# Kernel tuning notes

Hardware: AMD Instinct MI355X
Metric: run time of the kernel (lower is better)

Reference implementation:

```python
import jax, jax.numpy as jnp
import numpy as np

# LJ / module constants (from init_kwargs / defaults)
C = 1.0
RC = 1.0
P = 12
Q = 6
GAMMA = 0.1
MIN_R = 0.1

N_NODES = 100000
N_EDGES = 3200000
DIM = 3


def setup_inputs() -> dict:
    key = jax.random.key(0)
    k1, k2, k3, k4 = jax.random.split(key, 4)
    x = jax.random.normal(k1, (N_NODES, DIM), dtype=jnp.float32)
    v = jax.random.normal(k2, (N_NODES, DIM), dtype=jnp.float32)
    src = jax.random.randint(k3, (N_EDGES,), 0, N_NODES, dtype=jnp.int64)
    dst = jax.random.randint(k4, (N_EDGES,), 0, N_NODES, dtype=jnp.int64)
    return {"x": x, "v": v, "src": src, "dst": dst, "n_nodes": N_NODES}


def lj_force(r_in):
    # clamp r at MIN_R:  r = r_in if r_in > MIN_R else MIN_R
    r = jnp.where(r_in > MIN_R, r_in, MIN_R)
    s = RC / r
    return 4.0 * C * s**Q * (P * s**(P - Q) - Q) / r


def reference(x, v, src, dst, n_nodes):
    # gather edge endpoint positions; non-periodic distance: dst - src
    dr = x[dst] - x[src]                                  # [E, D]
    abs_dr = jnp.linalg.norm(dr, axis=-1, keepdims=True)  # [E, 1]
    # F.normalize(dr, dim=-1) -> dr / max(||dr||, eps)
    unit_dr = dr / jnp.maximum(abs_dr, 1e-12)             # [E, D]
    msg = lj_force(abs_dr) * unit_dr                      # [E, D]
    # scatter-sum messages into destination nodes
    acc = jax.ops.segment_sum(msg, dst, num_segments=n_nodes)  # [N, D]
    return acc - GAMMA * v
```

## Files before the change

kernel.cpp:

```cpp
#include <hip/hip_runtime.h>

#define GAMMA 0.1f
#define MIN_R 0.1f

#define NR 256
#define LOG_NR 8
#define RMAXB 512
#define SC_BS 4096
#define THR_S 512
#define THR_B 512
#define CAP 9216
#define NBMAX 1024

typedef unsigned int u32;

__device__ __forceinline__ u32 wave_incl_scan(u32 x) {
    #pragma unroll
    for (int d = 1; d < 64; d <<= 1) {
        u32 y = __shfl_up(x, d);
        if ((int)(threadIdx.x & 63) >= d) x += y;
    }
    return x;
}

__device__ __forceinline__ void lj_accum(float4 xd, float4 xs,
                                         float& ax, float& ay, float& az)
{
    float dx = xd.x - xs.x, dy = xd.y - xs.y, dz = xd.z - xs.z;
    float r2 = dx * dx + dy * dy + dz * dz;
    float rr = sqrtf(r2);
    float inv_norm = 1.0f / fmaxf(rr, 1e-12f);
    float rc = fmaxf(rr, MIN_R);
    float s1 = 1.0f / rc;
    float s2 = s1 * s1;
    float s6 = s2 * s2 * s2;
    float F = 4.0f * s6 * (12.0f * s6 - 6.0f) * s1;
    float sc = F * inv_norm;
    ax += sc * dx; ay += sc * dy; az += sc * dz;
}

__global__ __launch_bounds__(THR_S) void scatter_kernel(
    const float* __restrict__ x, const int* __restrict__ src,
    const int* __restrict__ dst, float4* __restrict__ xp,
    u32* __restrict__ pk1, u32* __restrict__ tab,
    int n_nodes, int n_edges, int NBv, int R)
{
    __shared__ u32 payload[SC_BS];
    __shared__ u32 hist[RMAXB], loff[RMAXB], lcur[RMAXB];
    __shared__ u32 wsb[8];
    const int b = blockIdx.x, t = threadIdx.x;

    for (int i = b * THR_S + t; i < n_nodes; i += NBv * THR_S)
        xp[i] = make_float4(x[3 * i + 0], x[3 * i + 1], x[3 * i + 2], 0.0f);

    const int s0 = b * SC_BS;
    const int n  = min(SC_BS, n_edges - s0);
    const int lim = s0 + n;

    hist[t] = 0u;
    __syncthreads();

    for (int e = s0 + t * 4; e < lim; e += THR_S * 4) {
        if (e + 3 < lim) {
            int4 d4 = *(const int4*)(dst + e);
            atomicAdd(&hist[(u32)d4.x >> LOG_NR], 1u);
            atomicAdd(&hist[(u32)d4.y >> LOG_NR], 1u);
            atomicAdd(&hist[(u32)d4.z >> LOG_NR], 1u);
            atomicAdd(&hist[(u32)d4.w >> LOG_NR], 1u);
        } else {
            for (int q = e; q < lim; ++q)
                atomicAdd(&hist[(u32)dst[q] >> LOG_NR], 1u);
        }
    }
    __syncthreads();

    {
        u32 h = hist[t];
        u32 inc = wave_incl_scan(h);
        if ((t & 63) == 63) wsb[t >> 6] = inc;
        __syncthreads();
        u32 pre = 0;
        #pragma unroll
        for (int w = 0; w < 8; ++w) if (w < (t >> 6)) pre += wsb[w];
        u32 ex = pre + inc - h;
        loff[t] = ex; lcur[t] = ex;
    }
    __syncthreads();

    for (int e = s0 + t * 4; e < lim; e += THR_S * 4) {
        if (e + 3 < lim) {
            int4 d4 = *(const int4*)(dst + e);
            int4 s4 = *(const int4*)(src + e);
            #pragma unroll
            for (int q = 0; q < 4; ++q) {
                u32 d = (u32)((q == 0) ? d4.x : (q == 1) ? d4.y : (q == 2) ? d4.z : d4.w);
                u32 sv = (u32)((q == 0) ? s4.x : (q == 1) ? s4.y : (q == 2) ? s4.z : s4.w);
                u32 r = d >> LOG_NR;
                u32 w = ((d & (NR - 1)) << 17) | sv;
                u32 slot = atomicAdd(&lcur[r], 1u);
                payload[slot] = w;
            }
        } else {
            for (int q = e; q < lim; ++q) {
                u32 d = (u32)dst[q];
                u32 sv = (u32)src[q];
                u32 r = d >> LOG_NR;
                u32 w = ((d & (NR - 1)) << 17) | sv;
                u32 slot = atomicAdd(&lcur[r], 1u);
                payload[slot] = w;
            }
        }
    }
    __syncthreads();

    for (int j = t; j < n; j += THR_S) pk1[s0 + j] = payload[j];
    for (int i = t; i < R; i += THR_S)
        tab[(size_t)b * R + i] = (loff[i] << 13) | hist[i];
}

__global__ __launch_bounds__(THR_B, 4) void binprocess_kernel(
    const float4* __restrict__ xp, const u32* __restrict__ pk1,
    const u32* __restrict__ tab, const float* __restrict__ v,
    float* __restrict__ out, int n_nodes, int NBv, int R)
{
    __shared__ u32 buf[CAP];
    __shared__ u32 sorted[CAP];
    __shared__ u32 segoff[NBMAX];
    __shared__ u32 hist[NR], cur[NR], ns[NR];
    __shared__ u32 wsb[8];
    __shared__ u32 shv[2];
    const int r = blockIdx.x, t = threadIdx.x;

    u32 c0 = 0, c1 = 0;
    if (t < NBv) c0 = tab[(size_t)t * R + r] & 8191u;
    if (t + THR_B < NBv) c1 = tab[(size_t)(t + THR_B) * R + r] & 8191u;
    u32 inc0 = wave_incl_scan(c0);
    if ((t & 63) == 63) wsb[t >> 6] = inc0;
    __syncthreads();
    u32 pre0 = 0;
    #pragma unroll
    for (int w = 0; w < 8; ++w) if (w < (t >> 6)) pre0 += wsb[w];
    u32 s0i = pre0 + inc0;
    if (t == THR_B - 1) shv[0] = s0i;
    __syncthreads();
    const u32 T0 = shv[0];
    u32 inc1 = wave_incl_scan(c1);
    if ((t & 63) == 63) wsb[t >> 6] = inc1;
    __syncthreads();
    u32 pre1 = 0;
    #pragma unroll
    for (int w = 0; w < 8; ++w) if (w < (t >> 6)) pre1 += wsb[w];
    u32 s1i = pre1 + inc1;
    if (t < NBv) segoff[t] = s0i - c0;
    if (t + THR_B < NBv) segoff[t + THR_B] = T0 + s1i - c1;
    if (t == THR_B - 1) shv[1] = T0 + s1i;
    __syncthreads();
    const u32 total = shv[1];

    if (total <= CAP) {
        if (t < NR) hist[t] = 0u;
        __syncthreads();
        for (int j = t; j < NBv; j += THR_B) {
            u32 w = tab[(size_t)j * R + r];
            int cnt = (int)(w & 8191u);
            const u32* seg = pk1 + (size_t)j * SC_BS + (w >> 13);
            u32 base = segoff[j];
            int k = 0;
            for (; k + 3 < cnt; k += 4) {
                u32 w0 = seg[k], w1 = seg[k + 1], w2 = seg[k + 2], w3 = seg[k + 3];
                buf[base + k] = w0; buf[base + k + 1] = w1;
                buf[base + k + 2] = w2; buf[base + k + 3] = w3;
                atomicAdd(&hist[w0 >> 17], 1u);
                atomicAdd(&hist[w1 >> 17], 1u);
                atomicAdd(&hist[w2 >> 17], 1u);
                atomicAdd(&hist[w3 >> 17], 1u);
            }
            for (; k < cnt; ++k) {
                u32 w0 = seg[k];
                buf[base + k] = w0;
                atomicAdd(&hist[w0 >> 17], 1u);
            }
        }
        __syncthreads();

        {
            u32 h = (t < NR) ? hist[t] : 0u;
            u32 inc = wave_incl_scan(h);
            if ((t & 63) == 63) wsb[t >> 6] = inc;
            __syncthreads();
            u32 pre = 0;
            #pragma unroll
            for (int w = 0; w < 8; ++w) if (w < (t >> 6)) pre += wsb[w];
            if (t < NR) {
                u32 ex = pre + inc - h;
                ns[t] = ex; cur[t] = ex;
            }
        }
        __syncthreads();

        for (int i = t; i < (int)total; i += THR_B) {
            u32 w = buf[i];
            u32 p = atomicAdd(&cur[w >> 17], 1u);
            sorted[p] = w & 0x1FFFFu;
        }
        __syncthreads();

        const int dl = t >> 1, half = t & 1;
        const int node = (r << LOG_NR) + dl;
        if (node < n_nodes) {
            const float4 xd = xp[node];
            const int ee0 = (int)ns[dl];
            const int ee1 = (dl < NR - 1) ? (int)ns[dl + 1] : (int)total;
            float ax = 0.f, ay = 0.f, az = 0.f;
            int e = ee0 + half;
            for (; e + 6 < ee1; e += 8) {
                u32 q0 = sorted[e], q1 = sorted[e + 2];
                u32 q2 = sorted[e + 4], q3 = sorted[e + 6];
                float4 a0 = xp[q0], a1 = xp[q1], a2 = xp[q2], a3 = xp[q3];
                lj_accum(xd, a0, ax, ay, az);
                lj_accum(xd, a1, ax, ay, az);
                lj_accum(xd, a2, ax, ay, az);
                lj_accum(xd, a3, ax, ay, az);
            }
            for (; e < ee1; e += 2) {
                float4 a = xp[sorted[e]];
                lj_accum(xd, a, ax, ay, az);
            }
            ax += __shfl_xor(ax, 1);
            ay += __shfl_xor(ay, 1);
            az += __shfl_xor(az, 1);
            if (half == 0) {
                out[3 * node + 0] = ax - GAMMA * v[3 * node + 0];
                out[3 * node + 1] = ay - GAMMA * v[3 * node + 1];
                out[3 * node + 2] = az - GAMMA * v[3 * node + 2];
            }
        }
    } else {
        float* acc = (float*)buf;
        for (int i = t; i < NR * 3; i += THR_B) acc[i] = 0.f;
        __syncthreads();
        for (int j = t; j < NBv; j += THR_B) {
            u32 w = tab[(size_t)j * R + r];
            int cnt = (int)(w & 8191u);
            const u32* seg = pk1 + (size_t)j * SC_BS + (w >> 13);
            for (int k = 0; k < cnt; ++k) {
                u32 w0 = seg[k];
                int u = (int)(w0 >> 17);
                int node = (r << LOG_NR) + u;
                float4 xs = xp[w0 & 0x1FFFFu];
                float4 xd = xp[node];
                float ax = 0.f, ay = 0.f, az = 0.f;
                lj_accum(xd, xs, ax, ay, az);
                unsafeAtomicAdd(&acc[3 * u + 0], ax);
                unsafeAtomicAdd(&acc[3 * u + 1], ay);
                unsafeAtomicAdd(&acc[3 * u + 2], az);
            }
        }
        __syncthreads();
        for (int i = t; i < NR; i += THR_B) {
            int node = (r << LOG_NR) + i;
            if (node < n_nodes) {
                out[3 * node + 0] = acc[3 * i + 0] - GAMMA * v[3 * node + 0];
                out[3 * node + 1] = acc[3 * i + 1] - GAMMA * v[3 * node + 1];
                out[3 * node + 2] = acc[3 * i + 2] - GAMMA * v[3 * node + 2];
            }
        }
    }
}

__global__ void init_out_kernel(const float* __restrict__ v,
                                float* __restrict__ out, int n) {
    int i = blockIdx.x * blockDim.x + threadIdx.x;
    if (i < n) out[i] = -GAMMA * v[i];
}

__global__ void edge_atomic_kernel(const float* __restrict__ x,
                                   const int* __restrict__ src,
                                   const int* __restrict__ dst,
                                   float* __restrict__ out, int n_edges) {
    int e = blockIdx.x * blockDim.x + threadIdx.x;
    if (e < n_edges) {
        const int s3 = 3 * src[e], d3 = 3 * dst[e];
        float dx = x[d3 + 0] - x[s3 + 0];
        float dy = x[d3 + 1] - x[s3 + 1];
        float dz = x[d3 + 2] - x[s3 + 2];
        float r2 = dx * dx + dy * dy + dz * dz;
        float rr = sqrtf(r2);
        float inv_norm = 1.0f / fmaxf(rr, 1e-12f);
        float rc = fmaxf(rr, MIN_R);
        float s1 = 1.0f / rc;
        float s2 = s1 * s1;
        float s6 = s2 * s2 * s2;
        float F = 4.0f * s6 * (12.0f * s6 - 6.0f) * s1;
        float sc = F * inv_norm;
        unsafeAtomicAdd(&out[d3 + 0], sc * dx);
        unsafeAtomicAdd(&out[d3 + 1], sc * dy);
        unsafeAtomicAdd(&out[d3 + 2], sc * dz);
    }
}

extern "C" void kernel_launch(void* const* d_in, const int* in_sizes, int n_in,
                              void* d_out, int out_size, void* d_ws, size_t ws_size,
                              hipStream_t stream) {
    const float* x   = (const float*)d_in[0];
    const float* v   = (const float*)d_in[1];
    const int*   src = (const int*)d_in[2];
    const int*   dst = (const int*)d_in[3];
    float* out = (float*)d_out;

    const int n_out   = out_size;
    const int n_nodes = out_size / 3;
    const int n_edges = in_sizes[2];
    const int R   = (n_nodes + NR - 1) / NR;
    const int NBv = (n_edges + SC_BS - 1) / SC_BS;

    size_t off = 0;
    auto take = [&off](size_t bytes) {
        size_t o = off;
        off = (off + bytes + 63) & ~(size_t)63;
        return o;
    };
    const size_t xp_o  = take((size_t)n_nodes * 16);
    const size_t tab_o = take((size_t)NBv * R * 4);
    const size_t pk1_o = take((size_t)NBv * SC_BS * 4);
    const size_t need = off;

    const int blk = 256;
    if (n_nodes <= (1 << 17) && R <= RMAXB && NBv <= NBMAX && need <= ws_size) {
        float4* xp = (float4*)((char*)d_ws + xp_o);
        u32* tab   = (u32*)((char*)d_ws + tab_o);
        u32* pk1   = (u32*)((char*)d_ws + pk1_o);

        scatter_kernel<<<NBv, THR_S, 0, stream>>>(x, src, dst, xp, pk1, tab,
                                                  n_nodes, n_edges, NBv, R);
        binprocess_kernel<<<R, THR_B, 0, stream>>>(xp, pk1, tab, v, out,
                                                   n_nodes, NBv, R);
    } else {
        init_out_kernel<<<(n_out + blk - 1) / blk, blk, 0, stream>>>(v, out, n_out);
        edge_atomic_kernel<<<(n_edges + blk - 1) / blk, blk, 0, stream>>>(
            x, src, dst, out, n_edges);
    }
}
```

Before: 115.3 us.

## Transpose bin table, drop staging buffer, and register-cache edges in scatter

```diff
diff --git a/kernel.cpp b/kernel.cpp
--- a/kernel.cpp
+++ b/kernel.cpp
@@ -10,7 +10,6 @@
 #define THR_S 512
 #define THR_B 512
 #define CAP 9216
-#define NBMAX 1024
 
 typedef unsigned int u32;
 
@@ -39,7 +38,7 @@
     ax += sc * dx; ay += sc * dy; az += sc * dz;
 }
 
-__global__ __launch_bounds__(THR_S) void scatter_kernel(
+__global__ __launch_bounds__(THR_S, 4) void scatter_kernel(
     const float* __restrict__ x, const int* __restrict__ src,
     const int* __restrict__ dst, float4* __restrict__ xp,
     u32* __restrict__ pk1, u32* __restrict__ tab,
@@ -57,21 +56,49 @@
     const int n  = min(SC_BS, n_edges - s0);
     const int lim = s0 + n;
 
+    u32 da[8], sa[8];
+    bool va[8];
+    {
+        const int eA = s0 + t * 4;
+        const int eB = eA + THR_S * 4;
+        if (eA + 3 < lim) {
+            int4 d4 = *(const int4*)(dst + eA);
+            int4 s4 = *(const int4*)(src + eA);
+            da[0] = (u32)d4.x; da[1] = (u32)d4.y; da[2] = (u32)d4.z; da[3] = (u32)d4.w;
+            sa[0] = (u32)s4.x; sa[1] = (u32)s4.y; sa[2] = (u32)s4.z; sa[3] = (u32)s4.w;
+            va[0] = va[1] = va[2] = va[3] = true;
+        } else {
+            #pragma unroll
+            for (int q = 0; q < 4; ++q) {
+                int qe = eA + q;
+                va[q] = qe < lim;
+                da[q] = va[q] ? (u32)dst[qe] : 0u;
+                sa[q] = va[q] ? (u32)src[qe] : 0u;
+            }
+        }
+        if (eB + 3 < lim) {
+            int4 d4 = *(const int4*)(dst + eB);
+            int4 s4 = *(const int4*)(src + eB);
+            da[4] = (u32)d4.x; da[5] = (u32)d4.y; da[6] = (u32)d4.z; da[7] = (u32)d4.w;
+            sa[4] = (u32)s4.x; sa[5] = (u32)s4.y; sa[6] = (u32)s4.z; sa[7] = (u32)s4.w;
+            va[4] = va[5] = va[6] = va[7] = true;
+        } else {
+            #pragma unroll
+            for (int q = 0; q < 4; ++q) {
+                int qe = eB + q;
+                va[4 + q] = qe < lim;
+                da[4 + q] = va[4 + q] ? (u32)dst[qe] : 0u;
+                sa[4 + q] = va[4 + q] ? (u32)src[qe] : 0u;
+            }
+        }
+    }
+
     hist[t] = 0u;
     __syncthreads();
 
-    for (int e = s0 + t * 4; e < lim; e += THR_S * 4) {
-        if (e + 3 < lim) {
-            int4 d4 = *(const int4*)(dst + e);
-            atomicAdd(&hist[(u32)d4.x >> LOG_NR], 1u);
-            atomicAdd(&hist[(u32)d4.y >> LOG_NR], 1u);
-            atomicAdd(&hist[(u32)d4.z >> LOG_NR], 1u);
-            atomicAdd(&hist[(u32)d4.w >> LOG_NR], 1u);
-        } else {
-            for (int q = e; q < lim; ++q)
-                atomicAdd(&hist[(u32)dst[q] >> LOG_NR], 1u);
-        }
-    }
+    #pragma unroll
+    for (int q = 0; q < 8; ++q)
+        if (va[q]) atomicAdd(&hist[da[q] >> LOG_NR], 1u);
     __syncthreads();
 
     {
@@ -87,35 +114,19 @@
     }
     __syncthreads();
 
-    for (int e = s0 + t * 4; e < lim; e += THR_S * 4) {
-        if (e + 3 < lim) {
-            int4 d4 = *(const int4*)(dst + e);
-            int4 s4 = *(const int4*)(src + e);
-            #pragma unroll
-            for (int q = 0; q < 4; ++q) {
-                u32 d = (u32)((q == 0) ? d4.x : (q == 1) ? d4.y : (q == 2) ? d4.z : d4.w);
-                u32 sv = (u32)((q == 0) ? s4.x : (q == 1) ? s4.y : (q == 2) ? s4.z : s4.w);
-                u32 r = d >> LOG_NR;
-                u32 w = ((d & (NR - 1)) << 17) | sv;
-                u32 slot = atomicAdd(&lcur[r], 1u);
-                payload[slot] = w;
-            }
-        } else {
-            for (int q = e; q < lim; ++q) {
-                u32 d = (u32)dst[q];
-                u32 sv = (u32)src[q];
-                u32 r = d >> LOG_NR;
-                u32 w = ((d & (NR - 1)) << 17) | sv;
-                u32 slot = atomicAdd(&lcur[r], 1u);
-                payload[slot] = w;
-            }
+    #pragma unroll
+    for (int q = 0; q < 8; ++q) {
+        if (va[q]) {
+            u32 r = da[q] >> LOG_NR;
+            u32 w = ((da[q] & (NR - 1)) << 17) | sa[q];
+            u32 slot = atomicAdd(&lcur[r], 1u);
+            payload[slot] = w;
         }
     }
     __syncthreads();
 
     for (int j = t; j < n; j += THR_S) pk1[s0 + j] = payload[j];
-    for (int i = t; i < R; i += THR_S)
-        tab[(size_t)b * R + i] = (loff[i] << 13) | hist[i];
+    if (t < R) tab[(size_t)t * NBv + b] = (loff[t] << 13) | hist[t];
 }
 
 __global__ __launch_bounds__(THR_B, 4) void binprocess_kernel(
@@ -123,85 +134,77 @@
     const u32* __restrict__ tab, const float* __restrict__ v,
     float* __restrict__ out, int n_nodes, int NBv, int R)
 {
-    __shared__ u32 buf[CAP];
     __shared__ u32 sorted[CAP];
-    __shared__ u32 segoff[NBMAX];
     __shared__ u32 hist[NR], cur[NR], ns[NR];
-    __shared__ u32 wsb[8];
-    __shared__ u32 shv[2];
+    __shared__ u32 wred[8];
     const int r = blockIdx.x, t = threadIdx.x;
-
-    u32 c0 = 0, c1 = 0;
-    if (t < NBv) c0 = tab[(size_t)t * R + r] & 8191u;
-    if (t + THR_B < NBv) c1 = tab[(size_t)(t + THR_B) * R + r] & 8191u;
-    u32 inc0 = wave_incl_scan(c0);
-    if ((t & 63) == 63) wsb[t >> 6] = inc0;
-    __syncthreads();
-    u32 pre0 = 0;
-    #pragma unroll
-    for (int w = 0; w < 8; ++w) if (w < (t >> 6)) pre0 += wsb[w];
-    u32 s0i = pre0 + inc0;
-    if (t == THR_B - 1) shv[0] = s0i;
-    __syncthreads();
-    const u32 T0 = shv[0];
-    u32 inc1 = wave_incl_scan(c1);
-    if ((t & 63) == 63) wsb[t >> 6] = inc1;
-    __syncthreads();
-    u32 pre1 = 0;
-    #pragma unroll
-    for (int w = 0; w < 8; ++w) if (w < (t >> 6)) pre1 += wsb[w];
-    u32 s1i = pre1 + inc1;
-    if (t < NBv) segoff[t] = s0i - c0;
-    if (t + THR_B < NBv) segoff[t + THR_B] = T0 + s1i - c1;
-    if (t == THR_B - 1) shv[1] = T0 + s1i;
-    __syncthreads();
-    const u32 total = shv[1];
+    const u32* __restrict__ trow = tab + (size_t)r * NBv;
+
+    u32 csum = 0;
+    for (int j = t; j < NBv; j += THR_B) csum += trow[j] & 8191u;
+    #pragma unroll
+    for (int d = 32; d > 0; d >>= 1) csum += __shfl_down(csum, d);
+    if ((t & 63) == 0) wred[t >> 6] = csum;
+    if (t < NR) hist[t] = 0u;
+    __syncthreads();
+    u32 total = 0;
+    #pragma unroll
+    for (int w = 0; w < 8; ++w) total += wred[w];
+    __syncthreads();
+
+    for (int j = t; j < NBv; j += THR_B) {
+        u32 w = trow[j];
+        int cnt = (int)(w & 8191u);
+        const u32* seg = pk1 + (size_t)j * SC_BS + (w >> 13);
+        int k = 0;
+        for (; k + 3 < cnt; k += 4) {
+            u32 w0 = seg[k], w1 = seg[k + 1], w2 = seg[k + 2], w3 = seg[k + 3];
+            atomicAdd(&hist[w0 >> 17], 1u);
+            atomicAdd(&hist[w1 >> 17], 1u);
+            atomicAdd(&hist[w2 >> 17], 1u);
+            atomicAdd(&hist[w3 >> 17], 1u);
+        }
+        for (; k < cnt; ++k) atomicAdd(&hist[seg[k] >> 17], 1u);
+    }
+    __syncthreads();
+
+    {
+        u32 h = (t < NR) ? hist[t] : 0u;
+        u32 inc = wave_incl_scan(h);
+        if ((t & 63) == 63 && t < NR) wred[t >> 6] = inc;
+        __syncthreads();
+        u32 pre = 0;
+        #pragma unroll
+        for (int w = 0; w < 4; ++w) if (w < (t >> 6)) pre += wred[w];
+        if (t < NR) {
+            u32 ex = pre + inc - h;
+            ns[t] = ex; cur[t] = ex;
+        }
+    }
+    __syncthreads();
 
     if (total <= CAP) {
-        if (t < NR) hist[t] = 0u;
-        __syncthreads();
         for (int j = t; j < NBv; j += THR_B) {
-            u32 w = tab[(size_t)j * R + r];
+            u32 w = trow[j];
             int cnt = (int)(w & 8191u);
             const u32* seg = pk1 + (size_t)j * SC_BS + (w >> 13);
-            u32 base = segoff[j];
             int k = 0;
             for (; k + 3 < cnt; k += 4) {
                 u32 w0 = seg[k], w1 = seg[k + 1], w2 = seg[k + 2], w3 = seg[k + 3];
-                buf[base + k] = w0; buf[base + k + 1] = w1;
-                buf[base + k + 2] = w2; buf[base + k + 3] = w3;
-                atomicAdd(&hist[w0 >> 17], 1u);
-                atomicAdd(&hist[w1 >> 17], 1u);
-                atomicAdd(&hist[w2 >> 17], 1u);
-                atomicAdd(&hist[w3 >> 17], 1u);
+                u32 p0 = atomicAdd(&cur[w0 >> 17], 1u);
+                u32 p1 = atomicAdd(&cur[w1 >> 17], 1u);
+                u32 p2 = atomicAdd(&cur[w2 >> 17], 1u);
+                u32 p3 = atomicAdd(&cur[w3 >> 17], 1u);
+                sorted[p0] = w0 & 0x1FFFFu;
+                sorted[p1] = w1 & 0x1FFFFu;
+                sorted[p2] = w2 & 0x1FFFFu;
+                sorted[p3] = w3 & 0x1FFFFu;
             }
             for (; k < cnt; ++k) {
                 u32 w0 = seg[k];
-                buf[base + k] = w0;
-                atomicAdd(&hist[w0 >> 17], 1u);
-            }
-        }
-        __syncthreads();
-
-        {
-            u32 h = (t < NR) ? hist[t] : 0u;
-            u32 inc = wave_incl_scan(h);
-            if ((t & 63) == 63) wsb[t >> 6] = inc;
-            __syncthreads();
-            u32 pre = 0;
-            #pragma unroll
-            for (int w = 0; w < 8; ++w) if (w < (t >> 6)) pre += wsb[w];
-            if (t < NR) {
-                u32 ex = pre + inc - h;
-                ns[t] = ex; cur[t] = ex;
-            }
-        }
-        __syncthreads();
-
-        for (int i = t; i < (int)total; i += THR_B) {
-            u32 w = buf[i];
-            u32 p = atomicAdd(&cur[w >> 17], 1u);
-            sorted[p] = w & 0x1FFFFu;
+                u32 p0 = atomicAdd(&cur[w0 >> 17], 1u);
+                sorted[p0] = w0 & 0x1FFFFu;
+            }
         }
         __syncthreads();
 
@@ -236,11 +239,11 @@
             }
         }
     } else {
-        float* acc = (float*)buf;
+        float* acc = (float*)sorted;
         for (int i = t; i < NR * 3; i += THR_B) acc[i] = 0.f;
         __syncthreads();
         for (int j = t; j < NBv; j += THR_B) {
-            u32 w = tab[(size_t)j * R + r];
+            u32 w = trow[j];
             int cnt = (int)(w & 8191u);
             const u32* seg = pk1 + (size_t)j * SC_BS + (w >> 13);
             for (int k = 0; k < cnt; ++k) {
@@ -321,12 +324,12 @@
         return o;
     };
     const size_t xp_o  = take((size_t)n_nodes * 16);
-    const size_t tab_o = take((size_t)NBv * R * 4);
+    const size_t tab_o = take((size_t)R * NBv * 4);
     const size_t pk1_o = take((size_t)NBv * SC_BS * 4);
     const size_t need = off;
 
     const int blk = 256;
-    if (n_nodes <= (1 << 17) && R <= RMAXB && NBv <= NBMAX && need <= ws_size) {
+    if (n_nodes <= (1 << 17) && R <= RMAXB && need <= ws_size) {
         float4* xp = (float4*)((char*)d_ws + xp_o);
         u32* tab   = (u32*)((char*)d_ws + tab_o);
         u32* pk1   = (u32*)((char*)d_ws + pk1_o);
```

Measured after the change: 125.3 us. 1.09x slower.

## Double scatter block size to halve segment count and simplify bin scan

Applied to the files above, without the earlier changes.

```diff
diff --git a/kernel.cpp b/kernel.cpp
--- a/kernel.cpp
+++ b/kernel.cpp
@@ -6,13 +6,14 @@
 #define NR 256
 #define LOG_NR 8
 #define RMAXB 512
-#define SC_BS 4096
+#define SC_BS 8192
 #define THR_S 512
 #define THR_B 512
 #define CAP 9216
-#define NBMAX 1024
+#define NBMAX 512
 
 typedef unsigned int u32;
+typedef unsigned short u16;
 
 __device__ __forceinline__ u32 wave_incl_scan(u32 x) {
     #pragma unroll
@@ -114,8 +115,7 @@
     __syncthreads();
 
     for (int j = t; j < n; j += THR_S) pk1[s0 + j] = payload[j];
-    for (int i = t; i < R; i += THR_S)
-        tab[(size_t)b * R + i] = (loff[i] << 13) | hist[i];
+    if (t < R) tab[(size_t)b * R + t] = (loff[t] << 16) | hist[t];
 }
 
 __global__ __launch_bounds__(THR_B, 4) void binprocess_kernel(
@@ -125,60 +125,50 @@
 {
     __shared__ u32 buf[CAP];
     __shared__ u32 sorted[CAP];
-    __shared__ u32 segoff[NBMAX];
-    __shared__ u32 hist[NR], cur[NR], ns[NR];
+    __shared__ u32 tabw[NBMAX];
+    __shared__ u16 segoff[NBMAX];
+    __shared__ u32 hist[NR], cur[NR];
     __shared__ u32 wsb[8];
-    __shared__ u32 shv[2];
+    __shared__ u32 shv[1];
     const int r = blockIdx.x, t = threadIdx.x;
 
-    u32 c0 = 0, c1 = 0;
-    if (t < NBv) c0 = tab[(size_t)t * R + r] & 8191u;
-    if (t + THR_B < NBv) c1 = tab[(size_t)(t + THR_B) * R + r] & 8191u;
-    u32 inc0 = wave_incl_scan(c0);
+    u32 w0 = 0;
+    if (t < NBv) w0 = tab[(size_t)t * R + r];
+    tabw[t] = w0;
+    u32 cnt0 = w0 & 0xFFFFu;
+    u32 inc0 = wave_incl_scan(cnt0);
     if ((t & 63) == 63) wsb[t >> 6] = inc0;
+    if (t < NR) hist[t] = 0u;
     __syncthreads();
     u32 pre0 = 0;
     #pragma unroll
     for (int w = 0; w < 8; ++w) if (w < (t >> 6)) pre0 += wsb[w];
-    u32 s0i = pre0 + inc0;
-    if (t == THR_B - 1) shv[0] = s0i;
-    __syncthreads();
-    const u32 T0 = shv[0];
-    u32 inc1 = wave_incl_scan(c1);
-    if ((t & 63) == 63) wsb[t >> 6] = inc1;
-    __syncthreads();
-    u32 pre1 = 0;
-    #pragma unroll
-    for (int w = 0; w < 8; ++w) if (w < (t >> 6)) pre1 += wsb[w];
-    u32 s1i = pre1 + inc1;
-    if (t < NBv) segoff[t] = s0i - c0;
-    if (t + THR_B < NBv) segoff[t + THR_B] = T0 + s1i - c1;
-    if (t == THR_B - 1) shv[1] = T0 + s1i;
-    __syncthreads();
-    const u32 total = shv[1];
+    u32 sincl = pre0 + inc0;
+    segoff[t] = (u16)(sincl - cnt0);
+    if (t == THR_B - 1) shv[0] = sincl;
+    __syncthreads();
+    const u32 total = shv[0];
 
     if (total <= CAP) {
-        if (t < NR) hist[t] = 0u;
-        __syncthreads();
-        for (int j = t; j < NBv; j += THR_B) {
-            u32 w = tab[(size_t)j * R + r];
-            int cnt = (int)(w & 8191u);
-            const u32* seg = pk1 + (size_t)j * SC_BS + (w >> 13);
-            u32 base = segoff[j];
+        if (t < NBv) {
+            u32 w = tabw[t];
+            int cnt = (int)(w & 0xFFFFu);
+            const u32* seg = pk1 + (size_t)t * SC_BS + (w >> 16);
+            u32 base = segoff[t];
             int k = 0;
             for (; k + 3 < cnt; k += 4) {
-                u32 w0 = seg[k], w1 = seg[k + 1], w2 = seg[k + 2], w3 = seg[k + 3];
-                buf[base + k] = w0; buf[base + k + 1] = w1;
-                buf[base + k + 2] = w2; buf[base + k + 3] = w3;
-                atomicAdd(&hist[w0 >> 17], 1u);
-                atomicAdd(&hist[w1 >> 17], 1u);
-                atomicAdd(&hist[w2 >> 17], 1u);
-                atomicAdd(&hist[w3 >> 17], 1u);
+                u32 a = seg[k], b2 = seg[k + 1], c = seg[k + 2], d = seg[k + 3];
+                buf[base + k] = a; buf[base + k + 1] = b2;
+                buf[base + k + 2] = c; buf[base + k + 3] = d;
+                atomicAdd(&hist[a >> 17], 1u);
+                atomicAdd(&hist[b2 >> 17], 1u);
+                atomicAdd(&hist[c >> 17], 1u);
+                atomicAdd(&hist[d >> 17], 1u);
             }
             for (; k < cnt; ++k) {
-                u32 w0 = seg[k];
-                buf[base + k] = w0;
-                atomicAdd(&hist[w0 >> 17], 1u);
+                u32 a = seg[k];
+                buf[base + k] = a;
+                atomicAdd(&hist[a >> 17], 1u);
             }
         }
         __syncthreads();
@@ -186,15 +176,12 @@
         {
             u32 h = (t < NR) ? hist[t] : 0u;
             u32 inc = wave_incl_scan(h);
-            if ((t & 63) == 63) wsb[t >> 6] = inc;
+            if ((t & 63) == 63 && t < NR) wsb[t >> 6] = inc;
             __syncthreads();
             u32 pre = 0;
             #pragma unroll
-            for (int w = 0; w < 8; ++w) if (w < (t >> 6)) pre += wsb[w];
-            if (t < NR) {
-                u32 ex = pre + inc - h;
-                ns[t] = ex; cur[t] = ex;
-            }
+            for (int w = 0; w < 4; ++w) if (w < (t >> 6)) pre += wsb[w];
+            if (t < NR) cur[t] = pre + inc - h;
         }
         __syncthreads();
 
@@ -209,8 +196,8 @@
         const int node = (r << LOG_NR) + dl;
         if (node < n_nodes) {
             const float4 xd = xp[node];
-            const int ee0 = (int)ns[dl];
-            const int ee1 = (dl < NR - 1) ? (int)ns[dl + 1] : (int)total;
+            const int ee1 = (int)cur[dl];
+            const int ee0 = dl ? (int)cur[dl - 1] : 0;
             float ax = 0.f, ay = 0.f, az = 0.f;
             int e = ee0 + half;
             for (; e + 6 < ee1; e += 8) {
@@ -239,10 +226,10 @@
         float* acc = (float*)buf;
         for (int i = t; i < NR * 3; i += THR_B) acc[i] = 0.f;
         __syncthreads();
-        for (int j = t; j < NBv; j += THR_B) {
-            u32 w = tab[(size_t)j * R + r];
-            int cnt = (int)(w & 8191u);
-            const u32* seg = pk1 + (size_t)j * SC_BS + (w >> 13);
+        if (t < NBv) {
+            u32 w = tabw[t];
+            int cnt = (int)(w & 0xFFFFu);
+            const u32* seg = pk1 + (size_t)t * SC_BS + (w >> 16);
             for (int k = 0; k < cnt; ++k) {
                 u32 w0 = seg[k];
                 int u = (int)(w0 >> 17);
```

After: 111.8 us. -3.0%, faster.
